# Optimization experiments

Measured on AMD Instinct MI355X. Metric: run time of the kernel, lower is better.

The kernel has to match this reference:

```python
import jax, jax.numpy as jnp
import numpy as np

B, T, C = 2, 4096, 1024
H = 16            # n_head (== n_groups == n_kv_heads)
HD = C // H       # head_dim = 64
W = 256           # window_size
ROPE_BASE = 10000.0


def _rope(x):
    # x: (B, H, T, HD); rotate interleaved pairs with position along axis 2
    t = x.shape[2]
    inv_freq = 1.0 / (ROPE_BASE ** (jnp.arange(0, HD, 2, dtype=jnp.float32) / HD))  # (HD/2,)
    freqs = jnp.arange(t, dtype=jnp.float32)[:, None] * inv_freq[None, :]           # (T, HD/2)
    cos = jnp.cos(freqs)[None, None].astype(x.dtype)
    sin = jnp.sin(freqs)[None, None].astype(x.dtype)
    x1, x2 = x[..., 0::2], x[..., 1::2]
    o1 = x1 * cos - x2 * sin
    o2 = x1 * sin + x2 * cos
    return jnp.stack([o1, o2], axis=-1).reshape(x.shape)


def setup_inputs() -> dict:
    key = jax.random.key(0)
    ks = jax.random.split(key, 5)
    s = 1.0 / np.sqrt(C)
    return {
        "x": jax.random.normal(ks[0], (B, T, C), dtype=jnp.float32),
        "wq": jax.random.normal(ks[1], (C, C), dtype=jnp.float32) * s,
        "wk": jax.random.normal(ks[2], (C, C), dtype=jnp.float32) * s,
        "wv": jax.random.normal(ks[3], (C, C), dtype=jnp.float32) * s,
        "wo": jax.random.normal(ks[4], (C, C), dtype=jnp.float32) * s,
    }


def reference(x, wq, wk, wv, wo):
    # projections (Linear stores (out, in) -> x @ w.T)
    q = jnp.einsum('btc,oc->bto', x, wq).reshape(B, T, H, HD).transpose(0, 2, 1, 3)
    k = jnp.einsum('btc,oc->bto', x, wk).reshape(B, T, H, HD).transpose(0, 2, 1, 3)
    v = jnp.einsum('btc,oc->bto', x, wv).reshape(B, T, H, HD).transpose(0, 2, 1, 3)

    q = _rope(q)
    k = _rope(k)

    nW = T // W
    qw = q.reshape(B, H, nW, W, HD)
    kw = k.reshape(B, H, nW, W, HD)
    vw = v.reshape(B, H, nW, W, HD)

    scale = 1.0 / jnp.sqrt(jnp.asarray(HD, dtype=q.dtype))
    att = jnp.einsum('bhnqd,bhnkd->bhnqk', qw, kw) * scale   # per-window, no causal mask
    att = jax.nn.softmax(att, axis=-1)
    yw = jnp.einsum('bhnqk,bhnkd->bhnqd', att, vw)

    y = yw.reshape(B, H, T, HD).transpose(0, 2, 1, 3).reshape(B, T, C)
    return jnp.einsum('btc,oc->bto', y, wo)
```

## Files before the change

### kernel.cpp

```cpp
#include <hip/hip_runtime.h>
#include <math.h>

typedef float f32x4 __attribute__((ext_vector_type(4)));
typedef __bf16 bf16x8 __attribute__((ext_vector_type(8)));
typedef unsigned short ushort_t;

#define MFMA16(a, b, c) __builtin_amdgcn_mfma_f32_16x16x32_bf16((a), (b), (c), 0, 0, 0)

static __device__ __forceinline__ ushort_t f2bf(float f) {
  union { float f; unsigned u; } v; v.f = f;
  unsigned u = v.u;
  return (ushort_t)((u + 0x7FFFu + ((u >> 16) & 1u)) >> 16);
}
static __device__ __forceinline__ float bf2f(ushort_t h) {
  union { unsigned u; float f; } v; v.u = ((unsigned)h) << 16;
  return v.f;
}
static __device__ __forceinline__ void gl_lds16(const void* g, void* lds_uniform) {
  __builtin_amdgcn_global_load_lds(
      (const __attribute__((address_space(1))) unsigned int*)g,
      (__attribute__((address_space(3))) unsigned int*)lds_uniform, 16, 0, 0);
}

__global__ void prep(const float* __restrict__ x,
                     const float* __restrict__ wq, const float* __restrict__ wk,
                     const float* __restrict__ wv, const float* __restrict__ wo,
                     ushort_t* __restrict__ Xb, ushort_t* __restrict__ Wqb,
                     ushort_t* __restrict__ Wkb, ushort_t* __restrict__ Wvb,
                     ushort_t* __restrict__ Wob, float2* __restrict__ cs) {
  const int bid = blockIdx.x;
  if (bid < 12288) {
    const float* src;
    ushort_t* dst;
    int i;
    if (bid < 8192) {
      src = x; dst = Xb;
      i = bid * 256 + threadIdx.x;
    } else {
      const int wi = (bid - 8192) >> 10;
      src = (wi == 0) ? wq : (wi == 1) ? wk : (wi == 2) ? wv : wo;
      dst = (wi == 0) ? Wqb : (wi == 1) ? Wkb : (wi == 2) ? Wvb : Wob;
      i = ((bid - 8192) & 1023) * 256 + threadIdx.x;
    }
    f32x4 v = ((const f32x4*)src)[i];
    ushort4 o;
    o.x = f2bf(v.x); o.y = f2bf(v.y); o.z = f2bf(v.z); o.w = f2bf(v.w);
    ((ushort4*)dst)[i] = o;
  } else {
    int idx = (bid - 12288) * 256 + threadIdx.x;
    int pos = idx >> 5, i = idx & 31;
    double inv = exp2(-(double)i * 0.41524101186092029);
    double th = (double)pos * inv;
    double s, c;
    sincos(th, &s, &c);
    cs[idx] = make_float2((float)c, (float)s);
  }
}

template <int OUTBF>
__global__ __launch_bounds__(512, 2) void gemm8(
    const ushort_t* __restrict__ A,
    const ushort_t* __restrict__ W0, const ushort_t* __restrict__ W1, const ushort_t* __restrict__ W2,
    void* __restrict__ C0, void* __restrict__ C1, void* __restrict__ C2,
    int K, int N) {
  __shared__ __align__(16) char smem[131072];
  const int z = blockIdx.z;
  const ushort_t* W = (z == 0) ? W0 : (z == 1 ? W1 : W2);
  void* Cv = (z == 0) ? C0 : (z == 1 ? C1 : C2);

  const int t = threadIdx.x;
  const int lane = t & 63;
  const int l15 = lane & 15, quad = lane >> 4;
  const int wave = t >> 6;
  const int wm = wave >> 2, wn = wave & 3;
  const int bm = blockIdx.x, bn = blockIdx.y;

  const int r0 = t >> 3;
  const int gc = (t & 7) ^ (r0 & 7);
  const ushort_t* AgB = A + (size_t)(bm * 256 + r0) * K + gc * 8;
  const ushort_t* WgB = W + (size_t)(bn * 256 + r0) * K + gc * 8;
  const size_t q64K = (size_t)64 * K;
  char* ldsw = smem + wave * 1024;

  const int sl0 = (quad ^ (l15 & 7)) * 16;
  const int aoff = (wm * 128 + l15) * 128 + sl0;
  const int boff = 32768 + (wn * 64 + l15) * 128 + sl0;

  const int KT = K >> 6;

  const f32x4 zero4 = {0.f, 0.f, 0.f, 0.f};
  f32x4 acc[8][4];
#pragma unroll
  for (int i = 0; i < 8; ++i)
#pragma unroll
    for (int j = 0; j < 4; ++j) acc[i][j] = zero4;

  auto stA = [&](int buf, int q, int kt) {
    gl_lds16(AgB + (size_t)q * q64K + (size_t)kt * 64, ldsw + buf * 65536 + q * 8192);
  };
  auto stB = [&](int buf, int q, int kt) {
    gl_lds16(WgB + (size_t)q * q64K + (size_t)kt * 64, ldsw + buf * 65536 + 32768 + q * 8192);
  };

#pragma unroll
  for (int q = 0; q < 4; ++q) stA(0, q, 0);
#pragma unroll
  for (int q = 0; q < 4; ++q) stB(0, q, 0);
#pragma unroll
  for (int q = 0; q < 4; ++q) stA(1, q, 1);
#pragma unroll
  for (int q = 0; q < 4; ++q) stB(1, q, 1);
  asm volatile("s_waitcnt vmcnt(8)" ::: "memory");
  __builtin_amdgcn_s_barrier();

  bf16x8 af[4][2], b01[2][2], b23[2][2];

  for (int j = 0; j < KT; ++j) {
    const int cb = j & 1;
    const char* bufb = smem + cb * 65536;
    const bool pf = (j + 2 < KT);
    const int k2 = j + 2;

#pragma unroll
    for (int m = 0; m < 4; ++m) {
      const int o = aoff + m * 2048;
      af[m][0] = *(const bf16x8*)(bufb + o);
      af[m][1] = *(const bf16x8*)(bufb + (o ^ 64));
    }
#pragma unroll
    for (int n = 0; n < 2; ++n) {
      const int o = boff + n * 2048;
      b01[n][0] = *(const bf16x8*)(bufb + o);
      b01[n][1] = *(const bf16x8*)(bufb + (o ^ 64));
    }
    __builtin_amdgcn_s_barrier();
    asm volatile("s_waitcnt lgkmcnt(0)" ::: "memory");
    __builtin_amdgcn_sched_barrier(0);
    __builtin_amdgcn_s_setprio(1);
#pragma unroll
    for (int m = 0; m < 4; ++m)
#pragma unroll
      for (int n = 0; n < 2; ++n) {
        acc[m][n] = MFMA16(af[m][0], b01[n][0], acc[m][n]);
        acc[m][n] = MFMA16(af[m][1], b01[n][1], acc[m][n]);
      }
    __builtin_amdgcn_s_setprio(0);
    __builtin_amdgcn_sched_barrier(0);
    __builtin_amdgcn_s_barrier();

#pragma unroll
    for (int n = 0; n < 2; ++n) {
      const int o = boff + (n + 2) * 2048;
      b23[n][0] = *(const bf16x8*)(bufb + o);
      b23[n][1] = *(const bf16x8*)(bufb + (o ^ 64));
    }
    if (pf) { stA(cb, 0, k2); stA(cb, 2, k2); }
    __builtin_amdgcn_s_barrier();
    asm volatile("s_waitcnt lgkmcnt(0)" ::: "memory");
    __builtin_amdgcn_sched_barrier(0);
    __builtin_amdgcn_s_setprio(1);
#pragma unroll
    for (int m = 0; m < 4; ++m)
#pragma unroll
      for (int n = 0; n < 2; ++n) {
        acc[m][n + 2] = MFMA16(af[m][0], b23[n][0], acc[m][n + 2]);
        acc[m][n + 2] = MFMA16(af[m][1], b23[n][1], acc[m][n + 2]);
      }
    __builtin_amdgcn_s_setprio(0);
    __builtin_amdgcn_sched_barrier(0);
    __builtin_amdgcn_s_barrier();

#pragma unroll
    for (int m = 0; m < 4; ++m) {
      const int o = aoff + (m + 4) * 2048;
      af[m][0] = *(const bf16x8*)(bufb + o);
      af[m][1] = *(const bf16x8*)(bufb + (o ^ 64));
    }
    if (pf) { stB(cb, 0, k2); stB(cb, 1, k2); }
    __builtin_amdgcn_s_barrier();
    asm volatile("s_waitcnt lgkmcnt(0)" ::: "memory");
    __builtin_amdgcn_sched_barrier(0);
    __builtin_amdgcn_s_setprio(1);
#pragma unroll
    for (int m = 0; m < 4; ++m)
#pragma unroll
      for (int n = 0; n < 2; ++n) {
        acc[m + 4][n] = MFMA16(af[m][0], b01[n][0], acc[m + 4][n]);
        acc[m + 4][n] = MFMA16(af[m][1], b01[n][1], acc[m + 4][n]);
      }
    __builtin_amdgcn_s_setprio(0);
    __builtin_amdgcn_sched_barrier(0);
    __builtin_amdgcn_s_barrier();

    if (pf) {
      stA(cb, 1, k2); stA(cb, 3, k2);
      stB(cb, 2, k2); stB(cb, 3, k2);
      asm volatile("s_waitcnt vmcnt(8)" ::: "memory");
    } else if (j + 1 < KT) {
      asm volatile("s_waitcnt vmcnt(0)" ::: "memory");
    }
    __builtin_amdgcn_s_barrier();
    __builtin_amdgcn_s_setprio(1);
#pragma unroll
    for (int m = 0; m < 4; ++m)
#pragma unroll
      for (int n = 0; n < 2; ++n) {
        acc[m + 4][n + 2] = MFMA16(af[m][0], b23[n][0], acc[m + 4][n + 2]);
        acc[m + 4][n + 2] = MFMA16(af[m][1], b23[n][1], acc[m + 4][n + 2]);
      }
    __builtin_amdgcn_s_setprio(0);
    __builtin_amdgcn_sched_barrier(0);
    __builtin_amdgcn_s_barrier();
  }

  const int rbase = bm * 256 + wm * 128 + quad * 4;
  const int cbase = bn * 256 + wn * 64 + l15;
#pragma unroll
  for (int m = 0; m < 8; ++m)
#pragma unroll
    for (int n = 0; n < 4; ++n)
#pragma unroll
      for (int r = 0; r < 4; ++r) {
        size_t idx = (size_t)(rbase + m * 16 + r) * N + (cbase + n * 16);
        if (OUTBF)
          ((ushort_t*)Cv)[idx] = f2bf(acc[m][n][r]);
        else
          ((float*)Cv)[idx] = acc[m][n][r];
      }
}

static __device__ __forceinline__ void rope8(const ushort_t* __restrict__ g,
                                             ushort_t* __restrict__ lds,
                                             const float2* __restrict__ cs4, float scale) {
  uint4 raw = *(const uint4*)g;
  unsigned rw[4] = {raw.x, raw.y, raw.z, raw.w};
  ushort_t o[8];
#pragma unroll
  for (int m = 0; m < 4; ++m) {
    float x1 = bf2f((ushort_t)(rw[m] & 0xffffu));
    float x2 = bf2f((ushort_t)(rw[m] >> 16));
    float2 sc = cs4[m];
    o[2 * m]     = f2bf((x1 * sc.x - x2 * sc.y) * scale);
    o[2 * m + 1] = f2bf((x1 * sc.y + x2 * sc.x) * scale);
  }
  uint4 w;
  w.x = (unsigned)o[0] | ((unsigned)o[1] << 16);
  w.y = (unsigned)o[2] | ((unsigned)o[3] << 16);
  w.z = (unsigned)o[4] | ((unsigned)o[5] << 16);
  w.w = (unsigned)o[6] | ((unsigned)o[7] << 16);
  *(uint4*)lds = w;
}

__global__ __launch_bounds__(256, 2) void attn(
    const ushort_t* __restrict__ Qb, const ushort_t* __restrict__ Kb,
    const ushort_t* __restrict__ Vb, ushort_t* __restrict__ Yb,
    const float2* __restrict__ cs) {
  __shared__ __align__(16) ushort_t smem[27648];
  ushort_t* Qs = smem;
  ushort_t* Ks = smem + 9216;
  ushort_t* Vt = smem;
  ushort_t* Pc = smem + 16896;

  const int t = threadIdx.x;
  const int lane = t & 63, wave = t >> 6;
  const int l15 = lane & 15, quad = lane >> 4;
  const int win = blockIdx.x >> 1, slice = blockIdx.x & 1;
  const int h = blockIdx.y, b = blockIdx.z;
  const int kBase = win * 256, qBase = kBase + slice * 128;
  const size_t gbase = ((size_t)b * 4096) * 1024 + h * 64;

  const int sr = t >> 3;
  const int c0 = (t & 7) * 8;

#pragma unroll
  for (int p = 0; p < 4; ++p) {
    int r = p * 32 + sr;
    rope8(Qb + gbase + (size_t)(qBase + r) * 1024 + c0, Qs + r * 72 + c0,
          cs + (qBase + r) * 32 + (c0 >> 1), 0.125f);
  }
#pragma unroll
  for (int p = 0; p < 8; ++p) {
    int r = p * 32 + sr;
    rope8(Kb + gbase + (size_t)(kBase + r) * 1024 + c0, Ks + r * 72 + c0,
          cs + (kBase + r) * 32 + (c0 >> 1), 1.0f);
  }
  __syncthreads();

  const int qw = wave * 32;
  const f32x4 zero4 = {0.f, 0.f, 0.f, 0.f};
  f32x4 S[2][16];
#pragma unroll
  for (int i = 0; i < 2; ++i)
#pragma unroll
    for (int j = 0; j < 16; ++j) S[i][j] = zero4;
#pragma unroll
  for (int ks = 0; ks < 2; ++ks) {
    bf16x8 a0 = *(const bf16x8*)&Qs[(qw + l15) * 72 + ks * 32 + quad * 8];
    bf16x8 a1 = *(const bf16x8*)&Qs[(qw + 16 + l15) * 72 + ks * 32 + quad * 8];
#pragma unroll
    for (int j = 0; j < 16; ++j) {
      bf16x8 bk = *(const bf16x8*)&Ks[(j * 16 + l15) * 72 + ks * 32 + quad * 8];
      S[0][j] = MFMA16(a0, bk, S[0][j]);
      S[1][j] = MFMA16(a1, bk, S[1][j]);
    }
  }

  float linv[2][4];
#pragma unroll
  for (int i = 0; i < 2; ++i)
#pragma unroll
    for (int r = 0; r < 4; ++r) {
      float mx = S[i][0][r];
#pragma unroll
      for (int j = 1; j < 16; ++j) mx = fmaxf(mx, S[i][j][r]);
      mx = fmaxf(mx, __shfl_xor(mx, 1));
      mx = fmaxf(mx, __shfl_xor(mx, 2));
      mx = fmaxf(mx, __shfl_xor(mx, 4));
      mx = fmaxf(mx, __shfl_xor(mx, 8));
      float sum = 0.f;
#pragma unroll
      for (int j = 0; j < 16; ++j) {
        float e = __expf(S[i][j][r] - mx);
        S[i][j][r] = e;
        sum += e;
      }
      sum += __shfl_xor(sum, 1);
      sum += __shfl_xor(sum, 2);
      sum += __shfl_xor(sum, 4);
      sum += __shfl_xor(sum, 8);
      linv[i][r] = 1.0f / sum;
    }
  __syncthreads();

#pragma unroll
  for (int p = 0; p < 8; ++p) {
    int k = p * 32 + sr;
    uint4 raw = *(const uint4*)(Vb + gbase + (size_t)(kBase + k) * 1024 + c0);
    ushort_t vv[8];
    vv[0] = raw.x & 0xffffu; vv[1] = raw.x >> 16;
    vv[2] = raw.y & 0xffffu; vv[3] = raw.y >> 16;
    vv[4] = raw.z & 0xffffu; vv[5] = raw.z >> 16;
    vv[6] = raw.w & 0xffffu; vv[7] = raw.w >> 16;
#pragma unroll
    for (int e = 0; e < 8; ++e) {
      int ee = (e + (t & 7)) & 7;
      Vt[(c0 + ee) * 264 + k] = vv[ee];
    }
  }

  auto writeP = [&](int kc) {
#pragma unroll
    for (int i = 0; i < 2; ++i)
#pragma unroll
      for (int jj = 0; jj < 4; ++jj) {
        int j = kc * 4 + jj;
#pragma unroll
        for (int r = 0; r < 4; ++r)
          Pc[(qw + i * 16 + quad * 4 + r) * 72 + jj * 16 + l15] = f2bf(S[i][j][r]);
      }
  };

  writeP(0);
  __syncthreads();

  f32x4 O[2][4];
#pragma unroll
  for (int i = 0; i < 2; ++i)
#pragma unroll
    for (int jd = 0; jd < 4; ++jd) O[i][jd] = zero4;

  for (int kc = 0; kc < 4; ++kc) {
#pragma unroll
    for (int ks = 0; ks < 2; ++ks) {
      bf16x8 a0 = *(const bf16x8*)&Pc[(qw + l15) * 72 + ks * 32 + quad * 8];
      bf16x8 a1 = *(const bf16x8*)&Pc[(qw + 16 + l15) * 72 + ks * 32 + quad * 8];
#pragma unroll
      for (int jd = 0; jd < 4; ++jd) {
        bf16x8 bv = *(const bf16x8*)&Vt[(jd * 16 + l15) * 264 + kc * 64 + ks * 32 + quad * 8];
        O[0][jd] = MFMA16(a0, bv, O[0][jd]);
        O[1][jd] = MFMA16(a1, bv, O[1][jd]);
      }
    }
    if (kc < 3) {
      __syncthreads();
      writeP(kc + 1);
      __syncthreads();
    }
  }

#pragma unroll
  for (int i = 0; i < 2; ++i)
#pragma unroll
    for (int jd = 0; jd < 4; ++jd)
#pragma unroll
      for (int r = 0; r < 4; ++r) {
        int row = qBase + qw + i * 16 + quad * 4 + r;
        int col = jd * 16 + l15;
        Yb[gbase + (size_t)row * 1024 + col] = f2bf(O[i][jd][r] * linv[i][r]);
      }
}

extern "C" void kernel_launch(void* const* d_in, const int* in_sizes, int n_in,
                              void* d_out, int out_size, void* d_ws, size_t ws_size,
                              hipStream_t stream) {
  (void)in_sizes; (void)n_in; (void)out_size; (void)ws_size;
  const float* x  = (const float*)d_in[0];
  const float* wq = (const float*)d_in[1];
  const float* wk = (const float*)d_in[2];
  const float* wv = (const float*)d_in[3];
  const float* wo = (const float*)d_in[4];

  char* ws = (char*)d_ws;
  ushort_t* Xb  = (ushort_t*)(ws);
  ushort_t* Wqb = (ushort_t*)(ws + 16777216);
  ushort_t* Wkb = Wqb + 1048576;
  ushort_t* Wvb = Wkb + 1048576;
  ushort_t* Wob = Wvb + 1048576;
  ushort_t* Qb  = (ushort_t*)(ws + 25165824);
  ushort_t* Kb  = Qb + 8388608;
  ushort_t* Vb  = Kb + 8388608;
  ushort_t* Yb  = Vb + 8388608;
  float2*   cs  = (float2*)(ws + 92274688);

  prep<<<dim3(12800), dim3(256), 0, stream>>>(x, wq, wk, wv, wo,
                                              Xb, Wqb, Wkb, Wvb, Wob, cs);

  gemm8<1><<<dim3(32, 4, 3), dim3(512), 0, stream>>>(
      Xb, Wqb, Wkb, Wvb, (void*)Qb, (void*)Kb, (void*)Vb, 1024, 1024);

  attn<<<dim3(32, 16, 2), dim3(256), 0, stream>>>(Qb, Kb, Vb, Yb, cs);

  gemm8<0><<<dim3(32, 4, 1), dim3(512), 0, stream>>>(
      Yb, Wob, Wob, Wob, d_out, d_out, d_out, 1024, 1024);
}
```

Baseline: 226.8 us.

## Shrink GEMM tile to 128x256 and software-pipeline LDS fragment reads

Result: faster. 205.6 us (-9.3%).

```diff
diff --git a/kernel.cpp b/kernel.cpp
--- a/kernel.cpp
+++ b/kernel.cpp
@@ -58,12 +58,12 @@
 }
 
 template <int OUTBF>
-__global__ __launch_bounds__(512, 2) void gemm8(
+__global__ __launch_bounds__(512, 2) void gemmp(
     const ushort_t* __restrict__ A,
     const ushort_t* __restrict__ W0, const ushort_t* __restrict__ W1, const ushort_t* __restrict__ W2,
     void* __restrict__ C0, void* __restrict__ C1, void* __restrict__ C2,
     int K, int N) {
-  __shared__ __align__(16) char smem[131072];
+  __shared__ __align__(16) char smem[98304];
   const int z = blockIdx.z;
   const ushort_t* W = (z == 0) ? W0 : (z == 1 ? W1 : W2);
   void* Cv = (z == 0) ? C0 : (z == 1 ? C1 : C2);
@@ -77,146 +77,164 @@
 
   const int r0 = t >> 3;
   const int gc = (t & 7) ^ (r0 & 7);
-  const ushort_t* AgB = A + (size_t)(bm * 256 + r0) * K + gc * 8;
-  const ushort_t* WgB = W + (size_t)(bn * 256 + r0) * K + gc * 8;
+  const ushort_t* Ag = A + (size_t)(bm * 128 + r0) * K + gc * 8;
+  const ushort_t* Wg = W + (size_t)(bn * 256 + r0) * K + gc * 8;
   const size_t q64K = (size_t)64 * K;
-  char* ldsw = smem + wave * 1024;
+  const int woff = wave * 1024;
 
   const int sl0 = (quad ^ (l15 & 7)) * 16;
-  const int aoff = (wm * 128 + l15) * 128 + sl0;
-  const int boff = 32768 + (wn * 64 + l15) * 128 + sl0;
+  const int aof = (wm * 64 + l15) * 128 + sl0;
+  const int bof = 16384 + (wn * 64 + l15) * 128 + sl0;
 
   const int KT = K >> 6;
 
   const f32x4 zero4 = {0.f, 0.f, 0.f, 0.f};
-  f32x4 acc[8][4];
-#pragma unroll
-  for (int i = 0; i < 8; ++i)
+  f32x4 acc[4][4];
+#pragma unroll
+  for (int i = 0; i < 4; ++i)
 #pragma unroll
     for (int j = 0; j < 4; ++j) acc[i][j] = zero4;
 
   auto stA = [&](int buf, int q, int kt) {
-    gl_lds16(AgB + (size_t)q * q64K + (size_t)kt * 64, ldsw + buf * 65536 + q * 8192);
+    gl_lds16(Ag + (size_t)q * q64K + (size_t)kt * 64,
+             smem + buf * 49152 + q * 8192 + woff);
   };
   auto stB = [&](int buf, int q, int kt) {
-    gl_lds16(WgB + (size_t)q * q64K + (size_t)kt * 64, ldsw + buf * 65536 + 32768 + q * 8192);
+    gl_lds16(Wg + (size_t)q * q64K + (size_t)kt * 64,
+             smem + buf * 49152 + 16384 + q * 8192 + woff);
   };
 
 #pragma unroll
-  for (int q = 0; q < 4; ++q) stA(0, q, 0);
-#pragma unroll
   for (int q = 0; q < 4; ++q) stB(0, q, 0);
-#pragma unroll
-  for (int q = 0; q < 4; ++q) stA(1, q, 1);
+  stA(0, 0, 0); stA(0, 1, 0);
 #pragma unroll
   for (int q = 0; q < 4; ++q) stB(1, q, 1);
-  asm volatile("s_waitcnt vmcnt(8)" ::: "memory");
+  stA(1, 0, 1); stA(1, 1, 1);
+  asm volatile("s_waitcnt vmcnt(6)" ::: "memory");
   __builtin_amdgcn_s_barrier();
 
-  bf16x8 af[4][2], b01[2][2], b23[2][2];
+  bf16x8 aX[2][2], aY[2][2], bX[2][2], bY[2][2];
+  {
+    const char* b0 = smem;
+#pragma unroll
+    for (int m = 0; m < 2; ++m) {
+      const int o = aof + m * 2048;
+      aX[m][0] = *(const bf16x8*)(b0 + o);
+      aX[m][1] = *(const bf16x8*)(b0 + (o ^ 64));
+    }
+#pragma unroll
+    for (int n = 0; n < 2; ++n) {
+      const int o = bof + n * 2048;
+      bX[n][0] = *(const bf16x8*)(b0 + o);
+      bX[n][1] = *(const bf16x8*)(b0 + (o ^ 64));
+    }
+  }
 
   for (int j = 0; j < KT; ++j) {
-    const int cb = j & 1;
-    const char* bufb = smem + cb * 65536;
-    const bool pf = (j + 2 < KT);
+    const int cb = j & 1, nb = cb ^ 1;
+    const char* bufc = smem + cb * 49152;
+    const char* bufn = smem + nb * 49152;
+    const bool st = (j + 2 < KT);
+    const bool rd = (j + 1 < KT);
     const int k2 = j + 2;
 
-#pragma unroll
-    for (int m = 0; m < 4; ++m) {
-      const int o = aoff + m * 2048;
-      af[m][0] = *(const bf16x8*)(bufb + o);
-      af[m][1] = *(const bf16x8*)(bufb + (o ^ 64));
-    }
+    asm volatile("s_waitcnt lgkmcnt(0)" ::: "memory");
+    __builtin_amdgcn_sched_barrier(0);
 #pragma unroll
     for (int n = 0; n < 2; ++n) {
-      const int o = boff + n * 2048;
-      b01[n][0] = *(const bf16x8*)(bufb + o);
-      b01[n][1] = *(const bf16x8*)(bufb + (o ^ 64));
-    }
+      const int o = bof + (n + 2) * 2048;
+      bY[n][0] = *(const bf16x8*)(bufc + o);
+      bY[n][1] = *(const bf16x8*)(bufc + (o ^ 64));
+    }
+    __builtin_amdgcn_sched_barrier(0);
+    __builtin_amdgcn_s_setprio(1);
+#pragma unroll
+    for (int m = 0; m < 2; ++m)
+#pragma unroll
+      for (int n = 0; n < 2; ++n) {
+        acc[m][n] = MFMA16(aX[m][0], bX[n][0], acc[m][n]);
+        acc[m][n] = MFMA16(aX[m][1], bX[n][1], acc[m][n]);
+      }
+    __builtin_amdgcn_s_setprio(0);
+    __builtin_amdgcn_sched_barrier(0);
+
+#pragma unroll
+    for (int m = 0; m < 2; ++m) {
+      const int o = aof + (m + 2) * 2048;
+      aY[m][0] = *(const bf16x8*)(bufc + o);
+      aY[m][1] = *(const bf16x8*)(bufc + (o ^ 64));
+    }
+    asm volatile("s_waitcnt lgkmcnt(4)" ::: "memory");
     __builtin_amdgcn_s_barrier();
+    if (st) {
+#pragma unroll
+      for (int q = 0; q < 4; ++q) stB(cb, q, k2);
+    }
+    __builtin_amdgcn_sched_barrier(0);
+    __builtin_amdgcn_s_setprio(1);
+#pragma unroll
+    for (int m = 0; m < 2; ++m)
+#pragma unroll
+      for (int n = 0; n < 2; ++n) {
+        acc[m][n + 2] = MFMA16(aX[m][0], bY[n][0], acc[m][n + 2]);
+        acc[m][n + 2] = MFMA16(aX[m][1], bY[n][1], acc[m][n + 2]);
+      }
+    __builtin_amdgcn_s_setprio(0);
+    __builtin_amdgcn_sched_barrier(0);
+
     asm volatile("s_waitcnt lgkmcnt(0)" ::: "memory");
+    if (st) {
+      asm volatile("s_waitcnt vmcnt(4)" ::: "memory");
+    } else if (rd) {
+      asm volatile("s_waitcnt vmcnt(0)" ::: "memory");
+    }
+    __builtin_amdgcn_s_barrier();
+    if (st) { stA(cb, 0, k2); stA(cb, 1, k2); }
+    if (rd) {
+#pragma unroll
+      for (int m = 0; m < 2; ++m) {
+        const int o = aof + m * 2048;
+        aX[m][0] = *(const bf16x8*)(bufn + o);
+        aX[m][1] = *(const bf16x8*)(bufn + (o ^ 64));
+      }
+    }
     __builtin_amdgcn_sched_barrier(0);
     __builtin_amdgcn_s_setprio(1);
 #pragma unroll
-    for (int m = 0; m < 4; ++m)
+    for (int m = 0; m < 2; ++m)
 #pragma unroll
       for (int n = 0; n < 2; ++n) {
-        acc[m][n] = MFMA16(af[m][0], b01[n][0], acc[m][n]);
-        acc[m][n] = MFMA16(af[m][1], b01[n][1], acc[m][n]);
+        acc[m + 2][n] = MFMA16(aY[m][0], bX[n][0], acc[m + 2][n]);
+        acc[m + 2][n] = MFMA16(aY[m][1], bX[n][1], acc[m + 2][n]);
       }
     __builtin_amdgcn_s_setprio(0);
     __builtin_amdgcn_sched_barrier(0);
-    __builtin_amdgcn_s_barrier();
-
-#pragma unroll
-    for (int n = 0; n < 2; ++n) {
-      const int o = boff + (n + 2) * 2048;
-      b23[n][0] = *(const bf16x8*)(bufb + o);
-      b23[n][1] = *(const bf16x8*)(bufb + (o ^ 64));
-    }
-    if (pf) { stA(cb, 0, k2); stA(cb, 2, k2); }
-    __builtin_amdgcn_s_barrier();
-    asm volatile("s_waitcnt lgkmcnt(0)" ::: "memory");
+
+    if (rd) {
+#pragma unroll
+      for (int n = 0; n < 2; ++n) {
+        const int o = bof + n * 2048;
+        bX[n][0] = *(const bf16x8*)(bufn + o);
+        bX[n][1] = *(const bf16x8*)(bufn + (o ^ 64));
+      }
+    }
     __builtin_amdgcn_sched_barrier(0);
     __builtin_amdgcn_s_setprio(1);
 #pragma unroll
-    for (int m = 0; m < 4; ++m)
+    for (int m = 0; m < 2; ++m)
 #pragma unroll
       for (int n = 0; n < 2; ++n) {
-        acc[m][n + 2] = MFMA16(af[m][0], b23[n][0], acc[m][n + 2]);
-        acc[m][n + 2] = MFMA16(af[m][1], b23[n][1], acc[m][n + 2]);
+        acc[m + 2][n + 2] = MFMA16(aY[m][0], bY[n][0], acc[m + 2][n + 2]);
+        acc[m + 2][n + 2] = MFMA16(aY[m][1], bY[n][1], acc[m + 2][n + 2]);
       }
     __builtin_amdgcn_s_setprio(0);
     __builtin_amdgcn_sched_barrier(0);
-    __builtin_amdgcn_s_barrier();
-
-#pragma unroll
-    for (int m = 0; m < 4; ++m) {
-      const int o = aoff + (m + 4) * 2048;
-      af[m][0] = *(const bf16x8*)(bufb + o);
-      af[m][1] = *(const bf16x8*)(bufb + (o ^ 64));
-    }
-    if (pf) { stB(cb, 0, k2); stB(cb, 1, k2); }
-    __builtin_amdgcn_s_barrier();
-    asm volatile("s_waitcnt lgkmcnt(0)" ::: "memory");
-    __builtin_amdgcn_sched_barrier(0);
-    __builtin_amdgcn_s_setprio(1);
-#pragma unroll
-    for (int m = 0; m < 4; ++m)
-#pragma unroll
-      for (int n = 0; n < 2; ++n) {
-        acc[m + 4][n] = MFMA16(af[m][0], b01[n][0], acc[m + 4][n]);
-        acc[m + 4][n] = MFMA16(af[m][1], b01[n][1], acc[m + 4][n]);
-      }
-    __builtin_amdgcn_s_setprio(0);
-    __builtin_amdgcn_sched_barrier(0);
-    __builtin_amdgcn_s_barrier();
-
-    if (pf) {
-      stA(cb, 1, k2); stA(cb, 3, k2);
-      stB(cb, 2, k2); stB(cb, 3, k2);
-      asm volatile("s_waitcnt vmcnt(8)" ::: "memory");
-    } else if (j + 1 < KT) {
-      asm volatile("s_waitcnt vmcnt(0)" ::: "memory");
-    }
-    __builtin_amdgcn_s_barrier();
-    __builtin_amdgcn_s_setprio(1);
-#pragma unroll
-    for (int m = 0; m < 4; ++m)
-#pragma unroll
-      for (int n = 0; n < 2; ++n) {
-        acc[m + 4][n + 2] = MFMA16(af[m][0], b23[n][0], acc[m + 4][n + 2]);
-        acc[m + 4][n + 2] = MFMA16(af[m][1], b23[n][1], acc[m + 4][n + 2]);
-      }
-    __builtin_amdgcn_s_setprio(0);
-    __builtin_amdgcn_sched_barrier(0);
-    __builtin_amdgcn_s_barrier();
-  }
-
-  const int rbase = bm * 256 + wm * 128 + quad * 4;
+  }
+
+  const int rbase = bm * 128 + wm * 64 + quad * 4;
   const int cbase = bn * 256 + wn * 64 + l15;
 #pragma unroll
-  for (int m = 0; m < 8; ++m)
+  for (int m = 0; m < 4; ++m)
 #pragma unroll
     for (int n = 0; n < 4; ++n)
 #pragma unroll
@@ -425,11 +443,11 @@
   prep<<<dim3(12800), dim3(256), 0, stream>>>(x, wq, wk, wv, wo,
                                               Xb, Wqb, Wkb, Wvb, Wob, cs);
 
-  gemm8<1><<<dim3(32, 4, 3), dim3(512), 0, stream>>>(
+  gemmp<1><<<dim3(64, 4, 3), dim3(512), 0, stream>>>(
       Xb, Wqb, Wkb, Wvb, (void*)Qb, (void*)Kb, (void*)Vb, 1024, 1024);
 
   attn<<<dim3(32, 16, 2), dim3(256), 0, stream>>>(Qb, Kb, Vb, Yb, cs);
 
-  gemm8<0><<<dim3(32, 4, 1), dim3(512), 0, stream>>>(
+  gemmp<0><<<dim3(64, 4, 1), dim3(512), 0, stream>>>(
       Yb, Wob, Wob, Wob, d_out, d_out, d_out, 1024, 1024);
 }
```
